# Performance work log

Measured on AMD Instinct MI355X. Metric: run time of the kernel, lower is better.

## Reference

```python
import jax, jax.numpy as jnp
import numpy as np

NUM_CLASSES = 21
BBOX_NUM = 2
BG_CLASS = 20          # nums_classes - 1
NMS_THR = 0.5
CLASS_OFFSET = 4096.0  # batched-NMS trick: shift boxes per class so IoU across classes is 0


def setup_inputs() -> dict:
    key = jax.random.key(0)
    # post-backbone feature map: C = bbox_num*5 + num_classes = 31, 28x28 grid (stride-32 on 896 image)
    features = jax.random.normal(key, (64, 31, 28, 28), dtype=jnp.float32)
    return {"features": features, "h_ori": 896, "w_ori": 896}


def _pairwise_iou(b):
    # b: [N, 4] (x1, y1, x2, y2) -> [N, N] IoU
    x1 = jnp.maximum(b[:, None, 0], b[None, :, 0])
    y1 = jnp.maximum(b[:, None, 1], b[None, :, 1])
    x2 = jnp.minimum(b[:, None, 2], b[None, :, 2])
    y2 = jnp.minimum(b[:, None, 3], b[None, :, 3])
    inter = jnp.clip(x2 - x1, 0.0) * jnp.clip(y2 - y1, 0.0)
    area = jnp.clip(b[:, 2] - b[:, 0], 0.0) * jnp.clip(b[:, 3] - b[:, 1], 0.0)
    union = area[:, None] + area[None, :] - inter
    return inter / jnp.maximum(union, 1e-9)


def _nms(boxes, scores, cats, valid):
    # class-aware greedy NMS on a single image; returns bool keep mask [N]
    N = boxes.shape[0]
    obox = boxes + (cats.astype(boxes.dtype) * CLASS_OFFSET)[:, None]
    s = jnp.where(valid, scores, -jnp.inf)
    order = jnp.argsort(-s)                 # descending score
    iou = _pairwise_iou(obox[order])        # [N, N] among sorted boxes
    idx = jnp.arange(N)

    def body(i, keep):
        ki = keep[i]
        suppress = (iou[i] > NMS_THR) & (idx > i) & ki
        return keep & ~suppress

    keep_sorted = jax.lax.fori_loop(0, N, body, valid[order])
    return jnp.zeros(N, bool).at[order].set(keep_sorted)


def reference(features, h_ori, w_ori):
    B, C, Hf, Wf = features.shape
    N = Hf * Wf
    # permute_and_flatten: [B, C, H, W] -> [B, H*W, C]
    x = features.transpose(0, 2, 3, 1).reshape(B, N, C)

    con_idx = jnp.arange(4, BBOX_NUM * 5, 5)            # confidence channels
    pred_conf = x[:, :, con_idx]                        # [B, N, bbox_num]
    pred_bbox = jax.nn.sigmoid(x[:, :, :BBOX_NUM * 5])  # [B, N, bbox_num*5]
    pred_class = jax.nn.softmax(x[:, :, BBOX_NUM * 5:], axis=-1)  # [B, N, num_classes]

    conf_max = jnp.max(pred_conf, axis=-1)              # [B, N]
    conf_arg = jnp.argmax(pred_conf, axis=-1)           # [B, N]
    con_prob = conf_max[..., None] * pred_class
    prob = jnp.max(con_prob, axis=-1)                   # [B, N]
    cat = jnp.argmax(con_prob, axis=-1)                 # [B, N]

    # Boxer.filter_bboxes: gather the 4 coords of the max-confidence box (offset = argmax*5)
    gidx = (conf_arg * 5)[..., None] + jnp.arange(4)    # [B, N, 4]
    box = jnp.take_along_axis(pred_bbox, gidx, axis=-1) # (x, y, w, h) in grid units

    # grid_cell_2_bbox (inverse of config_gt encoding), cell idx = row*Wf + col
    col = (jnp.arange(N) % Wf).astype(box.dtype)
    row = (jnp.arange(N) // Wf).astype(box.dtype)
    cx = (box[..., 0] + col) * (w_ori / Wf)
    cy = (box[..., 1] + row) * (h_ori / Hf)
    bw = box[..., 2] * w_ori
    bh = box[..., 3] * h_ori
    # convert center xywh -> corners
    boxes = jnp.stack([cx - bw / 2, cy - bh / 2, cx + bw / 2, cy + bh / 2], axis=-1)

    valid = cat != BG_CLASS                             # background filtering
    keep = jax.vmap(_nms)(boxes, prob, cat, valid)      # per-image NMS

    # fixed-shape packed output: [x1, y1, x2, y2, prob, cat, keep] -> [B, N, 7]
    out = jnp.concatenate(
        [boxes, prob[..., None], cat.astype(jnp.float32)[..., None],
         jnp.where(keep, 1.0, 0.0)[..., None]], axis=-1)
    return out
```

## Files before the change

kernel.cpp:

```cpp
#include <hip/hip_runtime.h>

#define BATCH 64
#define CH 31
#define HF 28
#define WF 28
#define NCELL 784
#define NCLS 21
#define BGCLS 20
#define CAP 128
#define NMS_THR 0.5f

__device__ __forceinline__ float bcast_f(float v, int l) {
    return __int_as_float(__builtin_amdgcn_readlane(__float_as_int(v), l));
}
__device__ __forceinline__ float fexp(float x) {
    return __expf(x);
}

__global__ __launch_bounds__(256)
void decode_kernel(const float* __restrict__ feat,
                   const int* __restrict__ hofp,
                   const int* __restrict__ wofp,
                   float* __restrict__ out,
                   float4* __restrict__ wbox,
                   unsigned long long* __restrict__ wkey)
{
    int gid = blockIdx.x * blockDim.x + threadIdx.x;
    if (gid >= BATCH * NCELL) return;
    int b = gid / NCELL;
    int n = gid - b * NCELL;

    const float* base = feat + (size_t)b * CH * NCELL + n;
    float x[CH];
#pragma unroll
    for (int c = 0; c < CH; ++c) x[c] = base[(size_t)c * NCELL];

    float c0 = x[4], c1 = x[9];
    int carg = (c1 > c0) ? 1 : 0;
    float cmax = fmaxf(c0, c1);

    float m = x[10];
#pragma unroll
    for (int k = 1; k < NCLS; ++k) m = fmaxf(m, x[10 + k]);
    float e[NCLS];
    float sum = 0.0f;
#pragma unroll
    for (int k = 0; k < NCLS; ++k) { e[k] = fexp(x[10 + k] - m); sum += e[k]; }
    float rinv = 1.0f / sum;

    float best = -INFINITY;
    int cat = 0;
#pragma unroll
    for (int k = 0; k < NCLS; ++k) {
        float cp = cmax * (e[k] * rinv);
        if (cp > best) { best = cp; cat = k; }
    }

    float rx = carg ? x[5] : x[0];
    float ry = carg ? x[6] : x[1];
    float rw = carg ? x[7] : x[2];
    float rh = carg ? x[8] : x[3];
    rx = 1.0f / (1.0f + fexp(-rx));
    ry = 1.0f / (1.0f + fexp(-ry));
    rw = 1.0f / (1.0f + fexp(-rw));
    rh = 1.0f / (1.0f + fexp(-rh));

    float w_ori = (float)(*wofp), h_ori = (float)(*hofp);
    float sw = w_ori / (float)WF, sh = h_ori / (float)HF;
    float col = (float)(n % WF), row = (float)(n / WF);
    float cx = (rx + col) * sw;
    float cy = (ry + row) * sh;
    float bw = rw * w_ori;
    float bh = rh * h_ori;
    float x1 = cx - bw * 0.5f, y1 = cy - bh * 0.5f;
    float x2 = cx + bw * 0.5f, y2 = cy + bh * 0.5f;

    float* o = out + (size_t)gid * 7;
    o[0] = x1; o[1] = y1; o[2] = x2; o[3] = y2;
    o[4] = best; o[5] = (float)cat; o[6] = 0.0f;

    float off = (float)cat * 4096.0f;
    wbox[gid] = make_float4(x1 + off, y1 + off, x2 + off, y2 + off);

    unsigned long long key = ~0ull;
    if (cat != BGCLS) {
        unsigned u = __float_as_uint(best);
        u = (u & 0x80000000u) ? ~u : (u | 0x80000000u);
        key = ((unsigned long long)(~u) << 15) |
              ((unsigned long long)cat << 10) | (unsigned)n;
    }
    wkey[gid] = key;
}

__global__ __launch_bounds__(256)
void nms_kernel(const float4* __restrict__ wbox,
                const unsigned long long* __restrict__ wkey,
                float* __restrict__ out)
{
    const int blk = blockIdx.x;
    const int b = blk / 5;
    const int wave = threadIdx.x >> 6;
    const int c = (blk - b * 5) * 4 + wave;
    const int lane = threadIdx.x & 63;

    __shared__ alignas(16) unsigned long long lb[4][CAP];
    __shared__ unsigned long long lb2[4][CAP];

    lb[wave][lane] = ~0ull;
    lb[wave][64 + lane] = ~0ull;

    int nacc = 0;
    const ulonglong2* wk2 = (const ulonglong2*)(wkey + (size_t)b * NCELL);
    unsigned long long low = (lane == 0) ? 0ull : ((1ull << lane) - 1ull);
#pragma unroll
    for (int it = 0; it < 7; ++it) {
        int ci = it * 128 + 2 * lane;
        unsigned long long ke = ~0ull, ko = ~0ull;
        if (ci < NCELL) {
            ulonglong2 kk = wk2[it * 64 + lane];
            ke = kk.x; ko = kk.y;
        }
        bool me = (((ke >> 10) & 31ull) == (unsigned long long)c);
        bool mo = (((ko >> 10) & 31ull) == (unsigned long long)c);
        unsigned long long balE = __ballot(me);
        unsigned long long balO = __ballot(mo);
        int pe = nacc + __popcll(balE & low) + __popcll(balO & low);
        int po = pe + (int)((balE >> lane) & 1ull);
        if (me && pe < CAP) lb[wave][pe] = ke;
        if (mo && po < CAP) lb[wave][po] = ko;
        nacc += (int)(__popcll(balE) + __popcll(balO));
    }
    int n = nacc > CAP ? CAP : nacc;
    if (n == 0) return;
    asm volatile("s_waitcnt lgkmcnt(0)" ::: "memory");

    bool ok0 = (lane < n);
    bool two = (n > 64);
    bool ok1 = two && ((64 + lane) < n);
    unsigned long long m0 = lb[wave][lane];
    unsigned long long m1 = lb[wave][64 + lane];

    int r0 = 0, r1 = 0;
    const ulonglong2* lp = (const ulonglong2*)&lb[wave][0];
    int half = (n + 1) >> 1;
    for (int j = 0; j < half; ++j) {
        ulonglong2 kk = lp[j];
        r0 += (kk.x < m0) ? 1 : 0; r0 += (kk.y < m0) ? 1 : 0;
        r1 += (kk.x < m1) ? 1 : 0; r1 += (kk.y < m1) ? 1 : 0;
    }
    if (ok0) lb2[wave][r0] = m0;
    if (ok1) lb2[wave][r1] = m1;
    asm volatile("s_waitcnt lgkmcnt(0)" ::: "memory");

    unsigned long long k0 = ok0 ? lb2[wave][lane] : ~0ull;
    unsigned long long k1 = ok1 ? lb2[wave][64 + lane] : ~0ull;
    int cell0 = (int)(k0 & 1023ull);
    int cell1 = (int)(k1 & 1023ull);

    const float4* wb = wbox + (size_t)b * NCELL;
    float4 B0 = wb[ok0 ? cell0 : 0];
    float a0 = fmaxf(B0.z - B0.x, 0.f) * fmaxf(B0.w - B0.y, 0.f);
    float4 B1 = make_float4(0.f, 0.f, 0.f, 0.f);
    float a1 = 0.f;
    if (two) {
        B1 = wb[ok1 ? cell1 : 0];
        a1 = fmaxf(B1.z - B1.x, 0.f) * fmaxf(B1.w - B1.y, 0.f);
    }

    unsigned long long s00 = 0ull, s01 = 0ull, s11 = 0ull;
    int n0 = (n < 64) ? n : 64;
    for (int s = 0; s < n0; ++s) {
        float ix1 = bcast_f(B0.x, s), iy1 = bcast_f(B0.y, s);
        float ix2 = bcast_f(B0.z, s), iy2 = bcast_f(B0.w, s);
        float ia  = bcast_f(a0, s);
        {
            float xx1 = fmaxf(ix1, B0.x), yy1 = fmaxf(iy1, B0.y);
            float xx2 = fminf(ix2, B0.z), yy2 = fminf(iy2, B0.w);
            float inter = fmaxf(xx2 - xx1, 0.f) * fmaxf(yy2 - yy1, 0.f);
            float uni = ia + a0 - inter;
            if ((inter / fmaxf(uni, 1e-9f)) > NMS_THR) s00 |= (1ull << s);
        }
        if (two) {
            float xx1 = fmaxf(ix1, B1.x), yy1 = fmaxf(iy1, B1.y);
            float xx2 = fminf(ix2, B1.z), yy2 = fminf(iy2, B1.w);
            float inter = fmaxf(xx2 - xx1, 0.f) * fmaxf(yy2 - yy1, 0.f);
            float uni = ia + a1 - inter;
            if ((inter / fmaxf(uni, 1e-9f)) > NMS_THR) s01 |= (1ull << s);
        }
    }
    if (two) {
        int n1 = n - 64;
        for (int s = 0; s < n1; ++s) {
            float ix1 = bcast_f(B1.x, s), iy1 = bcast_f(B1.y, s);
            float ix2 = bcast_f(B1.z, s), iy2 = bcast_f(B1.w, s);
            float ia  = bcast_f(a1, s);
            float xx1 = fmaxf(ix1, B1.x), yy1 = fmaxf(iy1, B1.y);
            float xx2 = fminf(ix2, B1.z), yy2 = fminf(iy2, B1.w);
            float inter = fmaxf(xx2 - xx1, 0.f) * fmaxf(yy2 - yy1, 0.f);
            float uni = ia + a1 - inter;
            if ((inter / fmaxf(uni, 1e-9f)) > NMS_THR) s11 |= (1ull << s);
        }
    }
    unsigned long long tri = (lane == 0) ? 0ull : ((1ull << lane) - 1ull);
    s00 &= tri;
    s11 &= tri;

    unsigned long long keep0 = (n >= 64) ? ~0ull : ((1ull << n) - 1ull);
    unsigned long long keep1 =
        two ? ((n >= 128) ? ~0ull : ((1ull << (n - 64)) - 1ull)) : 0ull;

    unsigned long long rem = keep0;
    while (rem) {
        int i = __builtin_ctzll(rem);
        rem &= rem - 1ull;
        keep0 &= ~__ballot(((s00 >> i) & 1ull) != 0ull);
        if (two) keep1 &= ~__ballot(((s01 >> i) & 1ull) != 0ull);
        rem &= keep0;
    }
    if (two) {
        unsigned long long rem1 = keep1;
        while (rem1) {
            int i = __builtin_ctzll(rem1);
            rem1 &= rem1 - 1ull;
            keep1 &= ~__ballot(((s11 >> i) & 1ull) != 0ull);
            rem1 &= keep1;
        }
    }

    if (ok0 && ((keep0 >> lane) & 1ull))
        out[((size_t)b * NCELL + cell0) * 7 + 6] = 1.0f;
    if (ok1 && ((keep1 >> lane) & 1ull))
        out[((size_t)b * NCELL + cell1) * 7 + 6] = 1.0f;
}

extern "C" void kernel_launch(void* const* d_in, const int* in_sizes, int n_in,
                              void* d_out, int out_size, void* d_ws, size_t ws_size,
                              hipStream_t stream) {
    const float* feat = (const float*)d_in[0];
    const int* h_ori  = (const int*)d_in[1];
    const int* w_ori  = (const int*)d_in[2];
    float* out = (float*)d_out;

    float4* wbox = (float4*)d_ws;
    unsigned long long* wkey =
        (unsigned long long*)((char*)d_ws + sizeof(float4) * BATCH * NCELL);

    int total = BATCH * NCELL;
    decode_kernel<<<(total + 255) / 256, 256, 0, stream>>>(
        feat, h_ori, w_ori, out, wbox, wkey);
    nms_kernel<<<BATCH * 5, 256, 0, stream>>>(wbox, wkey, out);
}
```

Measured before the change: 26.03 us.

## Fuse decode and per-class NMS into one kernel with shared-memory staging

Merges the decode and NMS kernels into one launch. Each 1024-thread block recomputes the decode for a whole image and keeps keys and boxes in LDS instead of a global workspace, then five waves each run NMS for one class. This removes a kernel launch and the global round-trip for the boxes and keys. The cost is that every image's decode runs four times (once per class-group block), and only the block that owns a cell's class writes that cell's output row, so there is no write race.

```diff
diff --git a/kernel.cpp b/kernel.cpp
--- a/kernel.cpp
+++ b/kernel.cpp
@@ -17,100 +17,98 @@
     return __expf(x);
 }
 
-__global__ __launch_bounds__(256)
-void decode_kernel(const float* __restrict__ feat,
-                   const int* __restrict__ hofp,
-                   const int* __restrict__ wofp,
-                   float* __restrict__ out,
-                   float4* __restrict__ wbox,
-                   unsigned long long* __restrict__ wkey)
-{
-    int gid = blockIdx.x * blockDim.x + threadIdx.x;
-    if (gid >= BATCH * NCELL) return;
-    int b = gid / NCELL;
-    int n = gid - b * NCELL;
-
-    const float* base = feat + (size_t)b * CH * NCELL + n;
-    float x[CH];
-#pragma unroll
-    for (int c = 0; c < CH; ++c) x[c] = base[(size_t)c * NCELL];
-
-    float c0 = x[4], c1 = x[9];
-    int carg = (c1 > c0) ? 1 : 0;
-    float cmax = fmaxf(c0, c1);
-
-    float m = x[10];
-#pragma unroll
-    for (int k = 1; k < NCLS; ++k) m = fmaxf(m, x[10 + k]);
-    float e[NCLS];
-    float sum = 0.0f;
-#pragma unroll
-    for (int k = 0; k < NCLS; ++k) { e[k] = fexp(x[10 + k] - m); sum += e[k]; }
-    float rinv = 1.0f / sum;
-
-    float best = -INFINITY;
-    int cat = 0;
-#pragma unroll
-    for (int k = 0; k < NCLS; ++k) {
-        float cp = cmax * (e[k] * rinv);
-        if (cp > best) { best = cp; cat = k; }
-    }
-
-    float rx = carg ? x[5] : x[0];
-    float ry = carg ? x[6] : x[1];
-    float rw = carg ? x[7] : x[2];
-    float rh = carg ? x[8] : x[3];
-    rx = 1.0f / (1.0f + fexp(-rx));
-    ry = 1.0f / (1.0f + fexp(-ry));
-    rw = 1.0f / (1.0f + fexp(-rw));
-    rh = 1.0f / (1.0f + fexp(-rh));
-
-    float w_ori = (float)(*wofp), h_ori = (float)(*hofp);
-    float sw = w_ori / (float)WF, sh = h_ori / (float)HF;
-    float col = (float)(n % WF), row = (float)(n / WF);
-    float cx = (rx + col) * sw;
-    float cy = (ry + row) * sh;
-    float bw = rw * w_ori;
-    float bh = rh * h_ori;
-    float x1 = cx - bw * 0.5f, y1 = cy - bh * 0.5f;
-    float x2 = cx + bw * 0.5f, y2 = cy + bh * 0.5f;
-
-    float* o = out + (size_t)gid * 7;
-    o[0] = x1; o[1] = y1; o[2] = x2; o[3] = y2;
-    o[4] = best; o[5] = (float)cat; o[6] = 0.0f;
-
-    float off = (float)cat * 4096.0f;
-    wbox[gid] = make_float4(x1 + off, y1 + off, x2 + off, y2 + off);
-
-    unsigned long long key = ~0ull;
-    if (cat != BGCLS) {
-        unsigned u = __float_as_uint(best);
-        u = (u & 0x80000000u) ? ~u : (u | 0x80000000u);
-        key = ((unsigned long long)(~u) << 15) |
-              ((unsigned long long)cat << 10) | (unsigned)n;
-    }
-    wkey[gid] = key;
-}
-
-__global__ __launch_bounds__(256)
-void nms_kernel(const float4* __restrict__ wbox,
-                const unsigned long long* __restrict__ wkey,
+__global__ __launch_bounds__(1024)
+void yolo_fused(const float* __restrict__ feat,
+                const int* __restrict__ hofp,
+                const int* __restrict__ wofp,
                 float* __restrict__ out)
 {
+    __shared__ alignas(16) unsigned long long keys[NCELL];
+    __shared__ float4 sbox[NCELL];
+    __shared__ alignas(16) unsigned long long lb[5][CAP];
+    __shared__ unsigned long long lb2[5][CAP];
+
     const int blk = blockIdx.x;
-    const int b = blk / 5;
-    const int wave = threadIdx.x >> 6;
-    const int c = (blk - b * 5) * 4 + wave;
-    const int lane = threadIdx.x & 63;
-
-    __shared__ alignas(16) unsigned long long lb[4][CAP];
-    __shared__ unsigned long long lb2[4][CAP];
+    const int b = blk >> 2;
+    const int h = blk & 3;
+    const int t = threadIdx.x;
+
+    if (t < NCELL) {
+        const float* base = feat + (size_t)b * CH * NCELL + t;
+        float x[CH];
+#pragma unroll
+        for (int c = 0; c < CH; ++c) x[c] = base[(size_t)c * NCELL];
+
+        float c0 = x[4], c1 = x[9];
+        int carg = (c1 > c0) ? 1 : 0;
+        float cmax = fmaxf(c0, c1);
+
+        float m = x[10];
+#pragma unroll
+        for (int k = 1; k < NCLS; ++k) m = fmaxf(m, x[10 + k]);
+        float sum = 0.0f;
+#pragma unroll
+        for (int k = 0; k < NCLS; ++k) sum += fexp(x[10 + k] - m);
+        float rinv = 1.0f / sum;
+
+        float best = -INFINITY;
+        int cat = 0;
+#pragma unroll
+        for (int k = 0; k < NCLS; ++k) {
+            float cp = cmax * (fexp(x[10 + k] - m) * rinv);
+            if (cp > best) { best = cp; cat = k; }
+        }
+
+        float rx = carg ? x[5] : x[0];
+        float ry = carg ? x[6] : x[1];
+        float rw = carg ? x[7] : x[2];
+        float rh = carg ? x[8] : x[3];
+        rx = 1.0f / (1.0f + fexp(-rx));
+        ry = 1.0f / (1.0f + fexp(-ry));
+        rw = 1.0f / (1.0f + fexp(-rw));
+        rh = 1.0f / (1.0f + fexp(-rh));
+
+        float w_ori = (float)(*wofp), h_ori = (float)(*hofp);
+        float sw = w_ori / (float)WF, sh = h_ori / (float)HF;
+        float col = (float)(t % WF), row = (float)(t / WF);
+        float cx = (rx + col) * sw;
+        float cy = (ry + row) * sh;
+        float bw = rw * w_ori;
+        float bh = rh * h_ori;
+        float x1 = cx - bw * 0.5f, y1 = cy - bh * 0.5f;
+        float x2 = cx + bw * 0.5f, y2 = cy + bh * 0.5f;
+
+        bool own = (cat >= 5 * h && cat < 5 * h + 5) || (h == 3 && cat == BGCLS);
+        if (own) {
+            float* o = out + ((size_t)b * NCELL + t) * 7;
+            o[0] = x1; o[1] = y1; o[2] = x2; o[3] = y2;
+            o[4] = best; o[5] = (float)cat; o[6] = 0.0f;
+        }
+
+        float off = (float)cat * 4096.0f;
+        sbox[t] = make_float4(x1 + off, y1 + off, x2 + off, y2 + off);
+
+        unsigned long long key = ~0ull;
+        if (cat != BGCLS) {
+            unsigned u = __float_as_uint(best);
+            u = (u & 0x80000000u) ? ~u : (u | 0x80000000u);
+            key = ((unsigned long long)(~u) << 15) |
+                  ((unsigned long long)cat << 10) | (unsigned)t;
+        }
+        keys[t] = key;
+    }
+    __syncthreads();
+
+    const int wave = t >> 6;
+    const int lane = t & 63;
+    if (wave >= 5) return;
+    const int c = 5 * h + wave;
 
     lb[wave][lane] = ~0ull;
     lb[wave][64 + lane] = ~0ull;
 
     int nacc = 0;
-    const ulonglong2* wk2 = (const ulonglong2*)(wkey + (size_t)b * NCELL);
+    const ulonglong2* wk2 = (const ulonglong2*)keys;
     unsigned long long low = (lane == 0) ? 0ull : ((1ull << lane) - 1ull);
 #pragma unroll
     for (int it = 0; it < 7; ++it) {
@@ -157,13 +155,12 @@
     int cell0 = (int)(k0 & 1023ull);
     int cell1 = (int)(k1 & 1023ull);
 
-    const float4* wb = wbox + (size_t)b * NCELL;
-    float4 B0 = wb[ok0 ? cell0 : 0];
+    float4 B0 = sbox[ok0 ? cell0 : 0];
     float a0 = fmaxf(B0.z - B0.x, 0.f) * fmaxf(B0.w - B0.y, 0.f);
     float4 B1 = make_float4(0.f, 0.f, 0.f, 0.f);
     float a1 = 0.f;
     if (two) {
-        B1 = wb[ok1 ? cell1 : 0];
+        B1 = sbox[ok1 ? cell1 : 0];
         a1 = fmaxf(B1.z - B1.x, 0.f) * fmaxf(B1.w - B1.y, 0.f);
     }
 
@@ -241,12 +238,5 @@
     const int* w_ori  = (const int*)d_in[2];
     float* out = (float*)d_out;
 
-    float4* wbox = (float4*)d_ws;
-    unsigned long long* wkey =
-        (unsigned long long*)((char*)d_ws + sizeof(float4) * BATCH * NCELL);
-
-    int total = BATCH * NCELL;
-    decode_kernel<<<(total + 255) / 256, 256, 0, stream>>>(
-        feat, h_ori, w_ori, out, wbox, wkey);
-    nms_kernel<<<BATCH * 5, 256, 0, stream>>>(wbox, wkey, out);
-}
+    yolo_fused<<<BATCH * 4, 1024, 0, stream>>>(feat, h_ori, w_ori, out);
+}
```

After: 21.90 us. 15.9% less time.
